# Optimization experiments

Measured on AMD Instinct MI355X. Metric: run time of the kernel, lower is better.

Reference implementation:

```python
import jax, jax.numpy as jnp
import numpy as np

MIN_K = 1
MAX_K = 10


def setup_inputs() -> dict:
    key = jax.random.key(0)
    k1, k2 = jax.random.split(key)
    query_features = jax.random.normal(k1, (256, 256, 32, 32), dtype=jnp.float32)
    support_features = jax.random.normal(k2, (512, 256, 32, 32), dtype=jnp.float32)
    return {"query_features": query_features, "support_features": support_features}


def _pairwise_euclidean(q, s):
    # torch.cdist(p=2): sqrt(||q||^2 + ||s||^2 - 2 q.s)
    q2 = jnp.sum(q * q, axis=1, keepdims=True)            # [Nq, 1]
    s2 = jnp.sum(s * s, axis=1)                           # [Ns]
    d2 = q2 + s2[None, :] - 2.0 * (q @ s.T)               # [Nq, Ns]
    return jnp.sqrt(jnp.maximum(d2, 0.0))


def reference(query_features, support_features):
    Nq = query_features.shape[0]
    q = query_features.reshape(Nq, -1)                    # [Nq, D]
    s = support_features.reshape(support_features.shape[0], -1)  # [Ns, D]

    dist = _pairwise_euclidean(q, s)                      # [Nq, Ns]

    # One top-k at MAX_K replaces the redundant per-k cdist+topk loop:
    # the per-k "loss" in optimize_k is mean of the k smallest-distance INDICES,
    # which is order-invariant, so prefix sums over sorted top-k suffice.
    _, idx = jax.lax.top_k(-dist, MAX_K)                  # [Nq, MAX_K] indices of k-NN (ascending distance)
    idx_f = idx.astype(jnp.float32)

    prefix = jnp.cumsum(jnp.sum(idx_f, axis=0))           # [MAX_K] sum of indices over first k cols
    ks = jnp.arange(1, MAX_K + 1, dtype=jnp.float32)
    losses = prefix / (Nq * ks)                           # mean index for each k
    best_k = jnp.argmin(losses[MIN_K - 1:]) + MIN_K       # traced scalar in [MIN_K, MAX_K]

    # threshold = mean of knn indices at best_k
    kmask = (jnp.arange(MAX_K) < best_k).astype(jnp.float32)  # [MAX_K]
    threshold = jnp.sum(idx_f * kmask[None, :]) / (Nq * best_k.astype(jnp.float32))

    # high_similarity mask: original expands [Nq, k] -> [Nq, D] (valid iff k==1),
    # i.e. a per-query boolean from the nearest-neighbor index vs threshold.
    qmask = (idx_f[:, 0] < threshold)                     # [Nq]

    # Original does data-dependent boolean gather; for static shapes we apply the
    # mask multiplicatively (zero out filtered queries).
    refined = q * qmask[:, None].astype(q.dtype)          # [Nq, D]
    return refined
```

## Files before the change

kernel.cpp:

```cpp
#include <hip/hip_runtime.h>
#include <cstdint>


typedef __attribute__((ext_vector_type(8))) __bf16 bf16x8;
typedef __attribute__((ext_vector_type(4))) float f32x4;
typedef __attribute__((ext_vector_type(4))) unsigned int uintx4;

#define KTOT 262144
#define MQ 256
#define NS 512
#define KSPLIT 128
#define KC 2048
#define BK 32
#define NSTEPS 64
#define BBASE 32768
#define BUFB 65536

__device__ inline unsigned int cvtpk_bf16(float a, float b) {
    unsigned int r;
    asm("v_cvt_pk_bf16_f32 %0, %1, %2" : "=v"(r) : "v"(a), "v"(b));
    return r;
}

__device__ inline void split2(float a, float b, unsigned int& h, unsigned int& l) {
    h = cvtpk_bf16(a, b);
    float ra = a - __uint_as_float(h << 16);
    float rb = b - __uint_as_float(h & 0xFFFF0000u);
    l = cvtpk_bf16(ra, rb);
}

__device__ inline void split8u(const float4& x, const float4& y, uintx4& h, uintx4& l) {
    unsigned int h0, h1, h2, h3, l0, l1, l2, l3;
    split2(x.x, x.y, h0, l0);
    split2(x.z, x.w, h1, l1);
    split2(y.x, y.y, h2, l2);
    split2(y.z, y.w, h3, l3);
    h = (uintx4){h0, h1, h2, h3};
    l = (uintx4){l0, l1, l2, l3};
}

#define LDF(OFF) (*(const bf16x8*)&Lds[(OFF)])

#define MM(MI, AH, AL, BH, BL, J)                                                        \
    acc[MI][J] = __builtin_amdgcn_mfma_f32_16x16x32_bf16(AH, BH, acc[MI][J], 0, 0, 0);   \
    acc[MI][J] = __builtin_amdgcn_mfma_f32_16x16x32_bf16(AH, BL, acc[MI][J], 0, 0, 0);   \
    acc[MI][J] = __builtin_amdgcn_mfma_f32_16x16x32_bf16(AL, BH, acc[MI][J], 0, 0, 0);

#define MMROW(MI, AH, AL)                                                                \
    MM(MI, AH, AL, bh0, bl0, 0) MM(MI, AH, AL, bh1, bl1, 1)                              \
    MM(MI, AH, AL, bh2, bl2, 2) MM(MI, AH, AL, bh3, bl3, 3)

#define PH_SYNC                                                                          \
    __builtin_amdgcn_s_barrier();                                                        \
    asm volatile("s_waitcnt lgkmcnt(0)" ::: "memory");                                   \
    __builtin_amdgcn_sched_barrier(0);

#define PH_END                                                                           \
    __builtin_amdgcn_sched_barrier(0);                                                   \
    __builtin_amdgcn_s_barrier();

__global__ __launch_bounds__(512, 2)
void k1_gemm(const float* __restrict__ Q, const float* __restrict__ S,
             float* __restrict__ Ppart, float* __restrict__ s2part)
{
    __shared__ __align__(16) unsigned char Lds[2 * BUFB];

    const int tid  = threadIdx.x;
    const int lane = tid & 63;
    const int w    = tid >> 6;
    const int wm   = w >> 2;
    const int wn   = w & 3;
    const int lr   = lane & 15;
    const int lk   = lane >> 4;

    const int phys  = blockIdx.x;
    const int xcd   = phys & 7;
    const int ord   = phys >> 3;
    const int chunk = xcd * 16 + (ord >> 1);
    const int ntile = ord & 1;
    const long k0   = (long)chunk * KC;

    const int rowh = tid >> 1;
    const int h    = tid & 1;
    const int e    = rowh & 7;
    const float* qsrc = Q + (long)rowh * KTOT + k0 + h * 16;
    const float* ssrc = S + (long)(ntile * 256 + rowh) * KTOT + k0 + h * 16;
    const int aw0 = rowh * 128 + (((2 * h + 0) ^ e) * 16);
    const int aw1 = rowh * 128 + (((2 * h + 1) ^ e) * 16);
    const int aw2 = rowh * 128 + (((2 * h + 4) ^ e) * 16);
    const int aw3 = rowh * 128 + (((2 * h + 5) ^ e) * 16);

    const int e2  = lr & 7;
    const int aHi = (wm * 128 + lr) * 128 + ((lk ^ e2) * 16);
    const int aLo = (wm * 128 + lr) * 128 + ((((lk + 4)) ^ e2) * 16);
    const int bHi = BBASE + (wn * 64 + lr) * 128 + ((lk ^ e2) * 16);
    const int bLo = BBASE + (wn * 64 + lr) * 128 + ((((lk + 4)) ^ e2) * 16);

    f32x4 acc[8][4];
#pragma unroll
    for (int i = 0; i < 8; ++i)
#pragma unroll
        for (int j = 0; j < 4; ++j)
            acc[i][j] = (f32x4){0.f, 0.f, 0.f, 0.f};

    float ssq = 0.f;
    float4 pa0, pa1, pa2, pa3, pb0, pb1, pb2, pb3;

#define LOADREGS {                                                         \
    pa0 = *(const float4*)(qsrc);      pa1 = *(const float4*)(qsrc + 4);   \
    pa2 = *(const float4*)(qsrc + 8);  pa3 = *(const float4*)(qsrc + 12);  \
    pb0 = *(const float4*)(ssrc);      pb1 = *(const float4*)(ssrc + 4);   \
    pb2 = *(const float4*)(ssrc + 8);  pb3 = *(const float4*)(ssrc + 12);  \
    qsrc += BK; ssrc += BK; }

#define SPLITSTORE(BASE) {                                                 \
    uintx4 u0, u1, u2, u3, v0, v1, v2, v3;                                 \
    split8u(pa0, pa1, u0, v0);                                             \
    split8u(pa2, pa3, u1, v1);                                             \
    split8u(pb0, pb1, u2, v2);                                             \
    split8u(pb2, pb3, u3, v3);                                             \
    ssq += pb0.x*pb0.x + pb0.y*pb0.y + pb0.z*pb0.z + pb0.w*pb0.w           \
         + pb1.x*pb1.x + pb1.y*pb1.y + pb1.z*pb1.z + pb1.w*pb1.w           \
         + pb2.x*pb2.x + pb2.y*pb2.y + pb2.z*pb2.z + pb2.w*pb2.w           \
         + pb3.x*pb3.x + pb3.y*pb3.y + pb3.z*pb3.z + pb3.w*pb3.w;          \
    *(uintx4*)&Lds[(BASE) + aw0] = u0;                                     \
    *(uintx4*)&Lds[(BASE) + aw1] = u1;                                     \
    *(uintx4*)&Lds[(BASE) + aw2] = v0;                                     \
    *(uintx4*)&Lds[(BASE) + aw3] = v1;                                     \
    *(uintx4*)&Lds[(BASE) + BBASE + aw0] = u2;                             \
    *(uintx4*)&Lds[(BASE) + BBASE + aw1] = u3;                             \
    *(uintx4*)&Lds[(BASE) + BBASE + aw2] = v2;                             \
    *(uintx4*)&Lds[(BASE) + BBASE + aw3] = v3; }

    LOADREGS
    SPLITSTORE(0)
    asm volatile("s_waitcnt lgkmcnt(0)" ::: "memory");
    __builtin_amdgcn_s_barrier();

    for (int s = 0; s < NSTEPS; ++s) {
        const int cur  = (s & 1) * BUFB;
        const int nxt  = cur ^ BUFB;
        const bool more = (s + 1 < NSTEPS);
        bf16x8 bh0, bh1, bh2, bh3, bl0, bl1, bl2, bl3;
        bf16x8 a0h, a0l, a1h, a1l;

        a0h = LDF(cur + aHi);          a0l = LDF(cur + aLo);
        a1h = LDF(cur + aHi + 2048);   a1l = LDF(cur + aLo + 2048);
        bh0 = LDF(cur + bHi);          bl0 = LDF(cur + bLo);
        bh1 = LDF(cur + bHi + 2048);   bl1 = LDF(cur + bLo + 2048);
        bh2 = LDF(cur + bHi + 4096);   bl2 = LDF(cur + bLo + 4096);
        bh3 = LDF(cur + bHi + 6144);   bl3 = LDF(cur + bLo + 6144);
        if (more) LOADREGS
        PH_SYNC
        __builtin_amdgcn_s_setprio(1);
        MMROW(0, a0h, a0l)
        MMROW(1, a1h, a1l)
        __builtin_amdgcn_s_setprio(0);
        PH_END

        a0h = LDF(cur + aHi + 4096);   a0l = LDF(cur + aLo + 4096);
        a1h = LDF(cur + aHi + 6144);   a1l = LDF(cur + aLo + 6144);
        PH_SYNC
        __builtin_amdgcn_s_setprio(1);
        MMROW(2, a0h, a0l)
        MMROW(3, a1h, a1l)
        __builtin_amdgcn_s_setprio(0);
        PH_END

        a0h = LDF(cur + aHi + 8192);   a0l = LDF(cur + aLo + 8192);
        a1h = LDF(cur + aHi + 10240);  a1l = LDF(cur + aLo + 10240);
        PH_SYNC
        __builtin_amdgcn_s_setprio(1);
        MMROW(4, a0h, a0l)
        MMROW(5, a1h, a1l)
        __builtin_amdgcn_s_setprio(0);
        PH_END

        a0h = LDF(cur + aHi + 12288);  a0l = LDF(cur + aLo + 12288);
        a1h = LDF(cur + aHi + 14336);  a1l = LDF(cur + aLo + 14336);
        PH_SYNC
        __builtin_amdgcn_s_setprio(1);
        MMROW(6, a0h, a0l)
        MMROW(7, a1h, a1l)
        __builtin_amdgcn_s_setprio(0);
        if (more) SPLITSTORE(nxt)
        asm volatile("s_waitcnt lgkmcnt(0)" ::: "memory");
        PH_END
    }
#undef LOADREGS
#undef SPLITSTORE

    float o = __shfl_xor(ssq, 1);
    if (h == 0)
        s2part[chunk * NS + ntile * 256 + rowh] = ssq + o;

    float* op = Ppart + (long)chunk * (MQ * NS);
#pragma unroll
    for (int mi = 0; mi < 8; ++mi)
#pragma unroll
        for (int nj = 0; nj < 4; ++nj) {
            int mb = wm * 128 + mi * 16 + lk * 4;
            int nn = ntile * 256 + wn * 64 + nj * 16 + lr;
#pragma unroll
            for (int r = 0; r < 4; ++r)
                op[(long)(mb + r) * NS + nn] = acc[mi][nj][r];
        }
}

__global__ __launch_bounds__(256)
void k2_topk(const float* __restrict__ Ppart, const float* __restrict__ s2part,
             int* __restrict__ idxb)
{
    __shared__ float d2s[NS];
    const int m = blockIdx.x;
    const int tid = threadIdx.x;
    for (int nn = tid; nn < NS; nn += 256) {
        float s2 = 0.f, p = 0.f;
        for (int c = 0; c < KSPLIT; ++c) {
            s2 += s2part[c * NS + nn];
            p  += Ppart[(long)c * (MQ * NS) + (long)m * NS + nn];
        }
        d2s[nn] = s2 - 2.f * p;
    }
    __syncthreads();
    if (tid < 64) {
        unsigned long long key[8];
#pragma unroll
        for (int j = 0; j < 8; ++j) {
            int n = tid * 8 + j;
            unsigned int u = __float_as_uint(d2s[n]);
            u = (u >> 31) ? ~u : (u | 0x80000000u);
            key[j] = ((unsigned long long)u << 32) | (unsigned int)n;
        }
        for (int it = 0; it < 10; ++it) {
            unsigned long long best = key[0];
#pragma unroll
            for (int j = 1; j < 8; ++j) best = key[j] < best ? key[j] : best;
            for (int d = 1; d < 64; d <<= 1) {
                unsigned long long o = __shfl_xor(best, d);
                best = o < best ? o : best;
            }
            if (tid == 0) idxb[m * 10 + it] = (int)(best & 0xFFFFFFFFu);
#pragma unroll
            for (int j = 0; j < 8; ++j) if (key[j] == best) key[j] = ~0ull;
        }
    }
}

__global__ __launch_bounds__(256)
void k3_thresh(const int* __restrict__ idxb, float* __restrict__ mask)
{
    __shared__ int colsum[10];
    __shared__ float thr;
    const int tid = threadIdx.x;
    if (tid < 10) {
        int s = 0;
        for (int m = 0; m < MQ; ++m) s += idxb[m * 10 + tid];
        colsum[tid] = s;
    }
    __syncthreads();
    if (tid == 0) {
        float pre = 0.f, best = 3.4e38f;
        for (int k = 1; k <= 10; ++k) {
            pre += (float)colsum[k - 1];
            float loss = pre / (256.0f * (float)k);
            if (loss < best) best = loss;
        }
        thr = best;
    }
    __syncthreads();
    if (tid < MQ) mask[tid] = ((float)idxb[tid * 10] < thr) ? 1.0f : 0.0f;
}

__global__ __launch_bounds__(256)
void k4_apply(const float* __restrict__ Q, const float* __restrict__ mask,
              float* __restrict__ out)
{
    long i = ((long)blockIdx.x * 256 + threadIdx.x) * 4;
    int row = (int)(i >> 18);
    float4 v = *(const float4*)(Q + i);
    float mm = mask[row];
    v.x *= mm; v.y *= mm; v.z *= mm; v.w *= mm;
    *(float4*)(out + i) = v;
}

extern "C" void kernel_launch(void* const* d_in, const int* in_sizes, int n_in,
                              void* d_out, int out_size, void* d_ws, size_t ws_size,
                              hipStream_t stream)
{
    const float* Q = (const float*)d_in[0];
    const float* S = (const float*)d_in[1];
    float* out = (float*)d_out;

    float* Ppart  = out;
    float* s2part = out + (long)KSPLIT * MQ * NS;
    int*   idxb   = (int*)(s2part + KSPLIT * NS);
    float* mask   = (float*)d_ws;

    hipLaunchKernelGGL(k1_gemm,  dim3(256),   dim3(512), 0, stream, Q, S, Ppart, s2part);
    hipLaunchKernelGGL(k2_topk,  dim3(MQ),    dim3(256), 0, stream, Ppart, s2part, idxb);
    hipLaunchKernelGGL(k3_thresh,dim3(1),     dim3(256), 0, stream, idxb, mask);
    hipLaunchKernelGGL(k4_apply, dim3(65536), dim3(256), 0, stream, Q, mask, out);
}
```

Before: 394.6 us.

## Replace four-phase barrier schedule with single-barrier loop and two-deep global prefetch

Removes the four barrier-synchronized phases per K-step and replaces them with one barrier per step. The split-store of the next tile now happens at the top of the iteration, and global loads are prefetched two steps ahead. The A/B LDS reads and MFMAs are left to the compiler to schedule. This cuts barrier overhead and lengthens the latency-hiding window for global loads. In exchange it drops the explicit setprio and interleaving control, and the extra register-held prefetch raises register pressure.

Result: faster. 383.2 us (-2.9%).

```diff
diff --git a/kernel.cpp b/kernel.cpp
--- a/kernel.cpp
+++ b/kernel.cpp
@@ -50,15 +50,6 @@
     MM(MI, AH, AL, bh0, bl0, 0) MM(MI, AH, AL, bh1, bl1, 1)                              \
     MM(MI, AH, AL, bh2, bl2, 2) MM(MI, AH, AL, bh3, bl3, 3)
 
-#define PH_SYNC                                                                          \
-    __builtin_amdgcn_s_barrier();                                                        \
-    asm volatile("s_waitcnt lgkmcnt(0)" ::: "memory");                                   \
-    __builtin_amdgcn_sched_barrier(0);
-
-#define PH_END                                                                           \
-    __builtin_amdgcn_sched_barrier(0);                                                   \
-    __builtin_amdgcn_s_barrier();
-
 __global__ __launch_bounds__(512, 2)
 void k1_gemm(const float* __restrict__ Q, const float* __restrict__ S,
              float* __restrict__ Ppart, float* __restrict__ s2part)
@@ -92,9 +83,9 @@
 
     const int e2  = lr & 7;
     const int aHi = (wm * 128 + lr) * 128 + ((lk ^ e2) * 16);
-    const int aLo = (wm * 128 + lr) * 128 + ((((lk + 4)) ^ e2) * 16);
+    const int aLo = (wm * 128 + lr) * 128 + (((lk + 4) ^ e2) * 16);
     const int bHi = BBASE + (wn * 64 + lr) * 128 + ((lk ^ e2) * 16);
-    const int bLo = BBASE + (wn * 64 + lr) * 128 + ((((lk + 4)) ^ e2) * 16);
+    const int bLo = BBASE + (wn * 64 + lr) * 128 + (((lk + 4) ^ e2) * 16);
 
     f32x4 acc[8][4];
 #pragma unroll
@@ -134,58 +125,32 @@
 
     LOADREGS
     SPLITSTORE(0)
+    LOADREGS
     asm volatile("s_waitcnt lgkmcnt(0)" ::: "memory");
     __builtin_amdgcn_s_barrier();
+    __builtin_amdgcn_sched_barrier(0);
 
     for (int s = 0; s < NSTEPS; ++s) {
-        const int cur  = (s & 1) * BUFB;
-        const int nxt  = cur ^ BUFB;
-        const bool more = (s + 1 < NSTEPS);
-        bf16x8 bh0, bh1, bh2, bh3, bl0, bl1, bl2, bl3;
-        bf16x8 a0h, a0l, a1h, a1l;
-
-        a0h = LDF(cur + aHi);          a0l = LDF(cur + aLo);
-        a1h = LDF(cur + aHi + 2048);   a1l = LDF(cur + aLo + 2048);
-        bh0 = LDF(cur + bHi);          bl0 = LDF(cur + bLo);
-        bh1 = LDF(cur + bHi + 2048);   bl1 = LDF(cur + bLo + 2048);
-        bh2 = LDF(cur + bHi + 4096);   bl2 = LDF(cur + bLo + 4096);
-        bh3 = LDF(cur + bHi + 6144);   bl3 = LDF(cur + bLo + 6144);
-        if (more) LOADREGS
-        PH_SYNC
-        __builtin_amdgcn_s_setprio(1);
-        MMROW(0, a0h, a0l)
-        MMROW(1, a1h, a1l)
-        __builtin_amdgcn_s_setprio(0);
-        PH_END
-
-        a0h = LDF(cur + aHi + 4096);   a0l = LDF(cur + aLo + 4096);
-        a1h = LDF(cur + aHi + 6144);   a1l = LDF(cur + aLo + 6144);
-        PH_SYNC
-        __builtin_amdgcn_s_setprio(1);
-        MMROW(2, a0h, a0l)
-        MMROW(3, a1h, a1l)
-        __builtin_amdgcn_s_setprio(0);
-        PH_END
-
-        a0h = LDF(cur + aHi + 8192);   a0l = LDF(cur + aLo + 8192);
-        a1h = LDF(cur + aHi + 10240);  a1l = LDF(cur + aLo + 10240);
-        PH_SYNC
-        __builtin_amdgcn_s_setprio(1);
-        MMROW(4, a0h, a0l)
-        MMROW(5, a1h, a1l)
-        __builtin_amdgcn_s_setprio(0);
-        PH_END
-
-        a0h = LDF(cur + aHi + 12288);  a0l = LDF(cur + aLo + 12288);
-        a1h = LDF(cur + aHi + 14336);  a1l = LDF(cur + aLo + 14336);
-        PH_SYNC
-        __builtin_amdgcn_s_setprio(1);
-        MMROW(6, a0h, a0l)
-        MMROW(7, a1h, a1l)
-        __builtin_amdgcn_s_setprio(0);
-        if (more) SPLITSTORE(nxt)
+        const int cur = (s & 1) * BUFB;
+        const int nxt = cur ^ BUFB;
+
+        if (s + 1 < NSTEPS) SPLITSTORE(nxt)
+        if (s + 2 < NSTEPS) LOADREGS
+
+        bf16x8 bh0 = LDF(cur + bHi);          bf16x8 bl0 = LDF(cur + bLo);
+        bf16x8 bh1 = LDF(cur + bHi + 2048);   bf16x8 bl1 = LDF(cur + bLo + 2048);
+        bf16x8 bh2 = LDF(cur + bHi + 4096);   bf16x8 bl2 = LDF(cur + bLo + 4096);
+        bf16x8 bh3 = LDF(cur + bHi + 6144);   bf16x8 bl3 = LDF(cur + bLo + 6144);
+#pragma unroll
+        for (int mi = 0; mi < 8; ++mi) {
+            bf16x8 ah = LDF(cur + aHi + mi * 2048);
+            bf16x8 al = LDF(cur + aLo + mi * 2048);
+            MMROW(mi, ah, al)
+        }
+
         asm volatile("s_waitcnt lgkmcnt(0)" ::: "memory");
-        PH_END
+        __builtin_amdgcn_s_barrier();
+        __builtin_amdgcn_sched_barrier(0);
     }
 #undef LOADREGS
 #undef SPLITSTORE
```
